# Kernel tuning notes

Hardware: AMD Instinct MI355X
Metric: run time of the kernel (lower is better)

Reference implementation:

```python
import jax, jax.numpy as jnp
import numpy as np

B, NINP, NCLS = 16384, 2048, 100


def setup_inputs() -> dict:
    key = jax.random.key(0)
    k1, k2, k3, k4, k5 = jax.random.split(key, 5)
    s = 1.0 / np.sqrt(NINP)
    return {
        "time_series": jax.random.normal(k1, (B, NINP), jnp.float32),
        "w_weight": jax.random.uniform(k2, (NINP, NINP), jnp.float32, -s, s),
        "w_bias": jax.random.uniform(k3, (NINP,), jnp.float32, -s, s),
        "fc_weight": jax.random.uniform(k4, (NCLS, NINP), jnp.float32, -s, s),
        "fc_bias": jax.random.uniform(k5, (NCLS,), jnp.float32, -s, s),
    }


def reference(time_series, w_weight, w_bias, fc_weight, fc_bias):
    # time_series: [B, N]
    n = time_series.shape[1]
    # gamma = cumsum(softmax(w(x), axis=1), axis=1): monotone warp in (0, 1]
    gamma = jnp.cumsum(jax.nn.softmax(time_series @ w_weight.T + w_bias, axis=1), axis=1)
    # Interp1d(linspace(0,1,N), x, gamma): per-row linear interpolation,
    # sampling each series at the warped time points gamma.
    xs = jnp.linspace(0.0, 1.0, n, dtype=time_series.dtype)  # shared knot grid
    warped = jax.vmap(lambda g, y: jnp.interp(g, xs, y))(gamma, time_series)  # [B, N]
    return warped @ fc_weight.T + fc_bias  # [B, nclasses]
```

## Files before the change

kernel.cpp:

```cpp
#include <hip/hip_runtime.h>
#include <hip/hip_bf16.h>

#define BROWS 16384
#define NDIM  2048
#define NCLS  100

typedef __attribute__((ext_vector_type(8))) __bf16 bf16x8;
typedef __attribute__((ext_vector_type(4))) float f32x4;
typedef __attribute__((ext_vector_type(16))) float f32x16;
typedef __attribute__((ext_vector_type(4))) unsigned short u16x4;
typedef __attribute__((ext_vector_type(8))) unsigned short u16x8;

__device__ __forceinline__ unsigned short f2bf(float f) {
    union { float f; unsigned int u; } v; v.f = f;
    unsigned int u = v.u;
    unsigned int r = (u + 0x7fffu + ((u >> 16) & 1u)) >> 16;
    return (unsigned short)r;
}
__device__ __forceinline__ float bf2f(unsigned short h) {
    union { unsigned int u; float f; } v; v.u = ((unsigned int)h) << 16;
    return v.f;
}

#define GLOAD_LDS(g, l) \
    __builtin_amdgcn_global_load_lds((const __attribute__((address_space(1))) void*)(g), \
                                     (__attribute__((address_space(3))) void*)(l), 16, 0, 0)

#define WAITCNT_VM(N) asm volatile("s_waitcnt vmcnt(" #N ")" ::: "memory")
#define WAITCNT_LGKM0() do { \
    asm volatile("s_waitcnt lgkmcnt(0)" ::: "memory"); \
    __builtin_amdgcn_sched_barrier(0); \
} while (0)
#define RAW_BARRIER() __builtin_amdgcn_s_barrier()

__global__ __launch_bounds__(256) void prep_kernel(const float4* __restrict__ x,
                                                   const float4* __restrict__ w,
                                                   u16x4* __restrict__ xhi, u16x4* __restrict__ xlo,
                                                   u16x4* __restrict__ whi, u16x4* __restrict__ wlo,
                                                   int n4x, int n4w)
{
    int i = blockIdx.x * 256 + threadIdx.x;
    const float4* src; u16x4 *hi, *lo; int idx;
    if (i < n4x) { src = x; hi = xhi; lo = xlo; idx = i; }
    else { idx = i - n4x; if (idx >= n4w) return; src = w; hi = whi; lo = wlo; }
    float4 v = src[idx];
    u16x4 h, l;
    h.x = f2bf(v.x); l.x = f2bf(v.x - bf2f(h.x));
    h.y = f2bf(v.y); l.y = f2bf(v.y - bf2f(h.y));
    h.z = f2bf(v.z); l.z = f2bf(v.z - bf2f(h.z));
    h.w = f2bf(v.w); l.w = f2bf(v.w - bf2f(h.w));
    hi[idx] = h; lo[idx] = l;
}

__global__ __launch_bounds__(256) void cvt_bf16_kernel(const float4* __restrict__ src,
                                                       u16x4* __restrict__ dst, int n4)
{
    int i = blockIdx.x * 256 + threadIdx.x;
    if (i >= n4) return;
    float4 v = src[i];
    u16x4 h;
    h.x = f2bf(v.x); h.y = f2bf(v.y); h.z = f2bf(v.z); h.w = f2bf(v.w);
    dst[i] = h;
}

__global__ __launch_bounds__(512) void gemm1_mfma_fused_kernel(
        const unsigned short* __restrict__ xhi,
        const unsigned short* __restrict__ xlo,
        const unsigned short* __restrict__ whi,
        const unsigned short* __restrict__ wlo,
        const float* __restrict__ bias,
        float* __restrict__ C)
{
    __shared__ unsigned short sAh[3 * 128 * 32];
    __shared__ unsigned short sAl[3 * 128 * 32];
    __shared__ unsigned short sBh[3 * 256 * 32];
    __shared__ unsigned short sBl[3 * 256 * 32];

    const int tid  = threadIdx.x;
    const int lane = tid & 63;
    const int w    = tid >> 6;
    const int wm   = w & 1;
    const int wn   = w >> 1;
    const int m0   = blockIdx.y * 128;
    const int n0   = blockIdx.x * 256;

    const int ra = tid >> 2;
    const int qa = (tid & 3) ^ ((ra >> 1) & 3);
    const size_t a_goff = (size_t)(m0 + ra) * NDIM + qa * 8;
    const int a_lb = (w * 64) * 8;

    size_t b_goff[2]; int b_lb[2];
#pragma unroll
    for (int t = 0; t < 2; t++) {
        const int c = t * 512 + tid;
        const int r = c >> 2;
        const int q = (c & 3) ^ ((r >> 1) & 3);
        b_goff[t] = (size_t)(n0 + r) * NDIM + q * 8;
        b_lb[t]   = (t * 512 + w * 64) * 8;
    }

    const int ln32 = lane & 31;
    const int lk2  = lane >> 5;
    int offA[2][2], offB[2][2];
#pragma unroll
    for (int i = 0; i < 2; i++)
#pragma unroll
        for (int ks = 0; ks < 2; ks++) {
            const int rfa = wm * 64 + i * 32 + ln32;
            offA[i][ks] = rfa * 32 + (((2 * ks + lk2) ^ ((rfa >> 1) & 3)) * 8);
            const int rfb = wn * 64 + i * 32 + ln32;
            offB[i][ks] = rfb * 32 + (((2 * ks + lk2) ^ ((rfb >> 1) & 3)) * 8);
        }

    f32x16 acc[2][2];
#pragma unroll
    for (int i = 0; i < 2; i++)
#pragma unroll
        for (int j = 0; j < 2; j++)
#pragma unroll
            for (int r = 0; r < 16; r++) acc[i][j][r] = 0.f;

#define G1_STAGE_ALL(AOFF, BOFF, KT) do { \
    GLOAD_LDS(xhi + a_goff + (KT), &sAh[(AOFF) + a_lb]); \
    GLOAD_LDS(xlo + a_goff + (KT), &sAl[(AOFF) + a_lb]); \
    GLOAD_LDS(whi + b_goff[0] + (KT), &sBh[(BOFF) + b_lb[0]]); \
    GLOAD_LDS(whi + b_goff[1] + (KT), &sBh[(BOFF) + b_lb[1]]); \
    GLOAD_LDS(wlo + b_goff[0] + (KT), &sBl[(BOFF) + b_lb[0]]); \
    GLOAD_LDS(wlo + b_goff[1] + (KT), &sBl[(BOFF) + b_lb[1]]); \
} while (0)

    G1_STAGE_ALL(0, 0, 0);
    G1_STAGE_ALL(4096, 8192, 32);
    WAITCNT_VM(6);
    RAW_BARRIER();

    int cA = 0, cB = 0;
    int sA = 2 * 4096, sB = 2 * 8192;

    for (int kt = 0; kt < NDIM; kt += 32) {
        const int skt = (kt + 64 < NDIM) ? kt + 64 : 0;

        {
            bf16x8 ah[2], al[2], bh[2], bl[2];
#pragma unroll
            for (int i = 0; i < 2; i++) {
                ah[i] = *(const bf16x8*)&sAh[cA + offA[i][0]];
                al[i] = *(const bf16x8*)&sAl[cA + offA[i][0]];
                bh[i] = *(const bf16x8*)&sBh[cB + offB[i][0]];
                bl[i] = *(const bf16x8*)&sBl[cB + offB[i][0]];
            }
            GLOAD_LDS(xhi + a_goff + skt, &sAh[sA + a_lb]);
            GLOAD_LDS(xlo + a_goff + skt, &sAl[sA + a_lb]);
            GLOAD_LDS(whi + b_goff[0] + skt, &sBh[sB + b_lb[0]]);
            RAW_BARRIER();
            WAITCNT_LGKM0();
            __builtin_amdgcn_s_setprio(1);
#pragma unroll
            for (int i = 0; i < 2; i++)
#pragma unroll
                for (int j = 0; j < 2; j++) {
                    acc[i][j] = __builtin_amdgcn_mfma_f32_32x32x16_bf16(ah[i], bh[j], acc[i][j], 0, 0, 0);
                    acc[i][j] = __builtin_amdgcn_mfma_f32_32x32x16_bf16(ah[i], bl[j], acc[i][j], 0, 0, 0);
                    acc[i][j] = __builtin_amdgcn_mfma_f32_32x32x16_bf16(al[i], bh[j], acc[i][j], 0, 0, 0);
                }
            __builtin_amdgcn_s_setprio(0);
            RAW_BARRIER();
        }

        {
            bf16x8 ah[2], al[2], bh[2], bl[2];
#pragma unroll
            for (int i = 0; i < 2; i++) {
                ah[i] = *(const bf16x8*)&sAh[cA + offA[i][1]];
                al[i] = *(const bf16x8*)&sAl[cA + offA[i][1]];
                bh[i] = *(const bf16x8*)&sBh[cB + offB[i][1]];
                bl[i] = *(const bf16x8*)&sBl[cB + offB[i][1]];
            }
            GLOAD_LDS(whi + b_goff[1] + skt, &sBh[sB + b_lb[1]]);
            GLOAD_LDS(wlo + b_goff[0] + skt, &sBl[sB + b_lb[0]]);
            GLOAD_LDS(wlo + b_goff[1] + skt, &sBl[sB + b_lb[1]]);
            WAITCNT_VM(6);
            RAW_BARRIER();
            WAITCNT_LGKM0();
            __builtin_amdgcn_s_setprio(1);
#pragma unroll
            for (int i = 0; i < 2; i++)
#pragma unroll
                for (int j = 0; j < 2; j++) {
                    acc[i][j] = __builtin_amdgcn_mfma_f32_32x32x16_bf16(ah[i], bh[j], acc[i][j], 0, 0, 0);
                    acc[i][j] = __builtin_amdgcn_mfma_f32_32x32x16_bf16(ah[i], bl[j], acc[i][j], 0, 0, 0);
                    acc[i][j] = __builtin_amdgcn_mfma_f32_32x32x16_bf16(al[i], bh[j], acc[i][j], 0, 0, 0);
                }
            __builtin_amdgcn_s_setprio(0);
            RAW_BARRIER();
        }

        cA += 4096; if (cA == 12288) cA = 0;
        cB += 8192; if (cB == 24576) cB = 0;
        sA += 4096; if (sA == 12288) sA = 0;
        sB += 8192; if (sB == 24576) sB = 0;
    }

#undef G1_STAGE_ALL

    float bb[2];
#pragma unroll
    for (int j = 0; j < 2; j++) bb[j] = bias[n0 + wn * 64 + j * 32 + ln32];
#pragma unroll
    for (int i = 0; i < 2; i++) {
#pragma unroll
        for (int j = 0; j < 2; j++) {
            const int n = n0 + wn * 64 + j * 32 + ln32;
#pragma unroll
            for (int reg = 0; reg < 16; reg++) {
                const int m = m0 + wm * 64 + i * 32 + (reg & 3) + 8 * (reg >> 2) + 4 * lk2;
                C[(size_t)m * NDIM + n] = acc[i][j][reg] + bb[j];
            }
        }
    }
}

#define SXI(i) ((i) + ((i) >> 5))

__global__ __launch_bounds__(256) void warp_bf16_kernel(const unsigned short* __restrict__ Xhi,
                                                        const unsigned short* __restrict__ Xlo,
                                                        const float* __restrict__ L,
                                                        unsigned short* __restrict__ Wout)
{
    const int N = NDIM;
    const int row = blockIdx.x;
    const int tid = threadIdx.x;
    const int lane = tid & 63;
    const int wave = tid >> 6;

    __shared__ float s_x[NDIM + NDIM / 32];
    __shared__ float s_red[4];
    __shared__ float s_wsum[4];

    const float* lrow = L + (size_t)row * N;

    float v[8];
    {
        float4 l0 = *(const float4*)(lrow + tid * 8);
        float4 l1 = *(const float4*)(lrow + tid * 8 + 4);
        v[0] = l0.x; v[1] = l0.y; v[2] = l0.z; v[3] = l0.w;
        v[4] = l1.x; v[5] = l1.y; v[6] = l1.z; v[7] = l1.w;
        u16x8 hx = *(const u16x8*)(Xhi + (size_t)row * N + tid * 8);
        u16x8 lx = *(const u16x8*)(Xlo + (size_t)row * N + tid * 8);
        float xv[8];
#pragma unroll
        for (int j = 0; j < 8; j++) xv[j] = bf2f(hx[j]) + bf2f(lx[j]);
        const int sb = SXI(tid * 8);
        *(float4*)&s_x[sb]     = make_float4(xv[0], xv[1], xv[2], xv[3]);
        *(float4*)&s_x[sb + 4] = make_float4(xv[4], xv[5], xv[6], xv[7]);
    }

    float mx = v[0];
#pragma unroll
    for (int j = 1; j < 8; j++) mx = fmaxf(mx, v[j]);
#pragma unroll
    for (int off = 32; off > 0; off >>= 1) mx = fmaxf(mx, __shfl_down(mx, off));
    if (lane == 0) s_red[wave] = mx;
    __syncthreads();
    mx = fmaxf(fmaxf(s_red[0], s_red[1]), fmaxf(s_red[2], s_red[3]));

    float c = 0.0f;
#pragma unroll
    for (int j = 0; j < 8; j++) {
        float e = __expf(v[j] - mx);
        c += e;
        v[j] = c;
    }

    float sc = c;
#pragma unroll
    for (int off = 1; off < 64; off <<= 1) {
        float t = __shfl_up(sc, off);
        if (lane >= off) sc += t;
    }
    if (lane == 63) s_wsum[wave] = sc;
    __syncthreads();
    float base = 0.0f, total = 0.0f;
#pragma unroll
    for (int w = 0; w < 4; w++) {
        float t = s_wsum[w];
        if (w < wave) base += t;
        total += t;
    }
    const float inv = 1.0f / total;
    const float prefix = base + (sc - c);

    u16x8 o;
#pragma unroll
    for (int j = 0; j < 8; j++) {
        float g = (prefix + v[j]) * inv;
        float pos = g * (float)(N - 1);
        pos = fminf(fmaxf(pos, 0.0f), (float)(N - 1));
        int i = (int)pos;
        if (i > N - 2) i = N - 2;
        float f = pos - (float)i;
        float x0 = s_x[SXI(i)];
        float x1 = s_x[SXI(i + 1)];
        o[j] = f2bf(fmaf(f, x1 - x0, x0));
    }
    *(u16x8*)(Wout + (size_t)row * N + tid * 8) = o;
}

__global__ __launch_bounds__(256) void gemm2_mfma_kernel(
        const unsigned short* __restrict__ Wp,
        const unsigned short* __restrict__ F,
        const float* __restrict__ fb,
        float* __restrict__ out)
{
    __shared__ unsigned short sA[2 * 32 * 64];
    __shared__ unsigned short sB[2 * 128 * 64];

    const int tid  = threadIdx.x;
    const int lane = tid & 63;
    const int w    = tid >> 6;
    const int m0   = blockIdx.x * 32;

    const int ar = tid >> 3, aq = tid & 7;
    const size_t a_goff = (size_t)(m0 + ar) * NDIM + ((aq ^ (ar & 7)) * 8);
    const int a_lb = (w * 64) * 8;

    size_t b_goff[4]; int b_lb[4];
#pragma unroll
    for (int t = 0; t < 4; t++) {
        const int c = t * 256 + tid;
        const int r = c >> 3, q = c & 7;
        b_goff[t] = (size_t)(r < NCLS ? r : NCLS - 1) * NDIM + ((q ^ (r & 7)) * 8);
        b_lb[t]   = (t * 256 + w * 64) * 8;
    }

    const int lm = lane & 15;
    const int lk = lane >> 4;
    int offA[2][2], offB[2][2];
#pragma unroll
    for (int i = 0; i < 2; i++)
#pragma unroll
        for (int ks = 0; ks < 2; ks++) {
            const int r = i * 16 + lm;
            offA[i][ks] = (r * 8 + ((ks * 4 + lk) ^ (r & 7))) * 8;
            const int rb = w * 32 + i * 16 + lm;
            offB[i][ks] = (rb * 8 + ((ks * 4 + lk) ^ (rb & 7))) * 8;
        }

    f32x4 acc[2][2];
#pragma unroll
    for (int i = 0; i < 2; i++)
#pragma unroll
        for (int j = 0; j < 2; j++) acc[i][j] = (f32x4){0.f, 0.f, 0.f, 0.f};

#define G2_STAGE(B, KT) do { \
    GLOAD_LDS(Wp + a_goff + (KT), &sA[(B) * 2048 + a_lb]); \
    _Pragma("unroll") \
    for (int t = 0; t < 4; t++) GLOAD_LDS(F + b_goff[t] + (KT), &sB[(B) * 8192 + b_lb[t]]); \
} while (0)

#define G2_COMPUTE(B) do { \
    _Pragma("unroll") \
    for (int ks = 0; ks < 2; ks++) { \
        bf16x8 af[2], bfr[2]; \
        _Pragma("unroll") \
        for (int i = 0; i < 2; i++) { \
            af[i]  = *(const bf16x8*)&sA[(B) * 2048 + offA[i][ks]]; \
            bfr[i] = *(const bf16x8*)&sB[(B) * 8192 + offB[i][ks]]; \
        } \
        _Pragma("unroll") \
        for (int i = 0; i < 2; i++) \
            _Pragma("unroll") \
            for (int j = 0; j < 2; j++) \
                acc[i][j] = __builtin_amdgcn_mfma_f32_16x16x32_bf16(af[i], bfr[j], acc[i][j], 0, 0, 0); \
    } \
} while (0)

    G2_STAGE(0, 0);

    for (int kt = 0; kt < NDIM; kt += 128) {
        G2_STAGE(1, kt + 64);
        WAITCNT_VM(5);
        RAW_BARRIER();
        G2_COMPUTE(0);
        RAW_BARRIER();
        G2_STAGE(0, (kt + 128 < NDIM) ? kt + 128 : 0);
        WAITCNT_VM(5);
        RAW_BARRIER();
        G2_COMPUTE(1);
        RAW_BARRIER();
    }

#undef G2_STAGE
#undef G2_COMPUTE

    const int cn = lane & 15;
    const int rg = lane >> 4;
#pragma unroll
    for (int i = 0; i < 2; i++) {
#pragma unroll
        for (int j = 0; j < 2; j++) {
            const int n = w * 32 + j * 16 + cn;
            if (n < NCLS) {
                const float bbn = fb[n];
#pragma unroll
                for (int reg = 0; reg < 4; reg++) {
                    const int m = m0 + i * 16 + rg * 4 + reg;
                    out[(size_t)m * NCLS + n] = acc[i][j][reg] + bbn;
                }
            }
        }
    }
}

__global__ __launch_bounds__(256) void gemm1_kernel(const float* __restrict__ X,
                                                    const float* __restrict__ W,
                                                    const float* __restrict__ bias,
                                                    float* __restrict__ C)
{
    const int K = NDIM;
    __shared__ float sA[16][128];
    __shared__ float sB[16][128];
    const int tid = threadIdx.x;
    const int tx = tid & 15;
    const int ty = tid >> 4;
    const int m0 = blockIdx.y * 128;
    const int n0 = blockIdx.x * 128;
    float acc[8][8];
#pragma unroll
    for (int i = 0; i < 8; i++)
#pragma unroll
        for (int j = 0; j < 8; j++) acc[i][j] = 0.0f;
    const int s_m = tid >> 1;
    const int s_c = (tid & 1) * 8;
    const float* Ag = X + (size_t)(m0 + s_m) * K + s_c;
    const float* Bg = W + (size_t)(n0 + s_m) * K + s_c;
    for (int kt = 0; kt < K; kt += 16) {
        float4 av0 = *(const float4*)(Ag + kt);
        float4 av1 = *(const float4*)(Ag + kt + 4);
        float4 bv0 = *(const float4*)(Bg + kt);
        float4 bv1 = *(const float4*)(Bg + kt + 4);
        __syncthreads();
        sA[s_c + 0][s_m] = av0.x; sA[s_c + 1][s_m] = av0.y;
        sA[s_c + 2][s_m] = av0.z; sA[s_c + 3][s_m] = av0.w;
        sA[s_c + 4][s_m] = av1.x; sA[s_c + 5][s_m] = av1.y;
        sA[s_c + 6][s_m] = av1.z; sA[s_c + 7][s_m] = av1.w;
        sB[s_c + 0][s_m] = bv0.x; sB[s_c + 1][s_m] = bv0.y;
        sB[s_c + 2][s_m] = bv0.z; sB[s_c + 3][s_m] = bv0.w;
        sB[s_c + 4][s_m] = bv1.x; sB[s_c + 5][s_m] = bv1.y;
        sB[s_c + 6][s_m] = bv1.z; sB[s_c + 7][s_m] = bv1.w;
        __syncthreads();
#pragma unroll
        for (int k = 0; k < 16; k++) {
            float4 a0 = *(const float4*)&sA[k][ty * 8];
            float4 a1 = *(const float4*)&sA[k][ty * 8 + 4];
            float4 b0 = *(const float4*)&sB[k][tx * 8];
            float4 b1 = *(const float4*)&sB[k][tx * 8 + 4];
            float a[8] = {a0.x, a0.y, a0.z, a0.w, a1.x, a1.y, a1.z, a1.w};
            float b[8] = {b0.x, b0.y, b0.z, b0.w, b1.x, b1.y, b1.z, b1.w};
#pragma unroll
            for (int i = 0; i < 8; i++)
#pragma unroll
                for (int j = 0; j < 8; j++)
                    acc[i][j] = fmaf(a[i], b[j], acc[i][j]);
        }
    }
    float bb[8];
#pragma unroll
    for (int j = 0; j < 8; j++) bb[j] = bias[n0 + tx * 8 + j];
#pragma unroll
    for (int i = 0; i < 8; i++) {
        const int m = m0 + ty * 8 + i;
        float* crow = C + (size_t)m * NDIM + n0 + tx * 8;
        *(float4*)(crow)     = make_float4(acc[i][0] + bb[0], acc[i][1] + bb[1],
                                           acc[i][2] + bb[2], acc[i][3] + bb[3]);
        *(float4*)(crow + 4) = make_float4(acc[i][4] + bb[4], acc[i][5] + bb[5],
                                           acc[i][6] + bb[6], acc[i][7] + bb[7]);
    }
}

__global__ __launch_bounds__(256) void warp_kernel_f32(const float* __restrict__ X,
                                                       float* __restrict__ L)
{
    const int N = NDIM;
    const int row = blockIdx.x;
    const int tid = threadIdx.x;
    const int lane = tid & 63;
    const int wave = tid >> 6;
    __shared__ float s_x[NDIM];
    __shared__ float s_red[4];
    __shared__ float s_wsum[4];
    float* lrow = L + (size_t)row * N;
    const float* xrow = X + (size_t)row * N;
    float v[8];
    {
        float4 l0 = *(const float4*)(lrow + tid * 8);
        float4 l1 = *(const float4*)(lrow + tid * 8 + 4);
        v[0] = l0.x; v[1] = l0.y; v[2] = l0.z; v[3] = l0.w;
        v[4] = l1.x; v[5] = l1.y; v[6] = l1.z; v[7] = l1.w;
        float4 x0 = *(const float4*)(xrow + tid * 8);
        float4 x1 = *(const float4*)(xrow + tid * 8 + 4);
        *(float4*)&s_x[tid * 8]     = x0;
        *(float4*)&s_x[tid * 8 + 4] = x1;
    }
    float mx = v[0];
#pragma unroll
    for (int j = 1; j < 8; j++) mx = fmaxf(mx, v[j]);
#pragma unroll
    for (int off = 32; off > 0; off >>= 1) mx = fmaxf(mx, __shfl_down(mx, off));
    if (lane == 0) s_red[wave] = mx;
    __syncthreads();
    mx = fmaxf(fmaxf(s_red[0], s_red[1]), fmaxf(s_red[2], s_red[3]));
    float c = 0.0f;
#pragma unroll
    for (int j = 0; j < 8; j++) {
        float e = __expf(v[j] - mx);
        c += e;
        v[j] = c;
    }
    float sc = c;
#pragma unroll
    for (int off = 1; off < 64; off <<= 1) {
        float t = __shfl_up(sc, off);
        if (lane >= off) sc += t;
    }
    if (lane == 63) s_wsum[wave] = sc;
    __syncthreads();
    float base = 0.0f, total = 0.0f;
#pragma unroll
    for (int w = 0; w < 4; w++) {
        float t = s_wsum[w];
        if (w < wave) base += t;
        total += t;
    }
    const float inv = 1.0f / total;
    const float prefix = base + (sc - c);
    float w8[8];
#pragma unroll
    for (int j = 0; j < 8; j++) {
        float g = (prefix + v[j]) * inv;
        float pos = g * (float)(N - 1);
        pos = fminf(fmaxf(pos, 0.0f), (float)(N - 1));
        int i = (int)pos;
        if (i > N - 2) i = N - 2;
        float f = pos - (float)i;
        w8[j] = fmaf(f, s_x[i + 1] - s_x[i], s_x[i]);
    }
    *(float4*)(lrow + tid * 8)     = make_float4(w8[0], w8[1], w8[2], w8[3]);
    *(float4*)(lrow + tid * 8 + 4) = make_float4(w8[4], w8[5], w8[6], w8[7]);
}

__global__ __launch_bounds__(256) void gemm2_kernel(const float* __restrict__ Wp,
                                                    const float* __restrict__ F,
                                                    const float* __restrict__ fb,
                                                    float* __restrict__ out)
{
    const int K = NDIM;
    __shared__ float sA[16][64];
    __shared__ float sB[16][128];
    const int tid = threadIdx.x;
    const int tx = tid & 15;
    const int ty = tid >> 4;
    const int m0 = blockIdx.x * 64;
    float acc[4][8];
#pragma unroll
    for (int i = 0; i < 4; i++)
#pragma unroll
        for (int j = 0; j < 8; j++) acc[i][j] = 0.0f;
    const int a_m = tid >> 2;
    const int a_c = (tid & 3) * 4;
    const int b_n = tid >> 1;
    const int b_c = (tid & 1) * 8;
    const bool bvalid = (b_n < NCLS);
    const float* Ag = Wp + (size_t)(m0 + a_m) * K + a_c;
    const float* Bg = F + (size_t)b_n * K + b_c;
    for (int kt = 0; kt < K; kt += 16) {
        float4 av = *(const float4*)(Ag + kt);
        float4 bv0 = make_float4(0.f, 0.f, 0.f, 0.f);
        float4 bv1 = make_float4(0.f, 0.f, 0.f, 0.f);
        if (bvalid) {
            bv0 = *(const float4*)(Bg + kt);
            bv1 = *(const float4*)(Bg + kt + 4);
        }
        __syncthreads();
        sA[a_c + 0][a_m] = av.x; sA[a_c + 1][a_m] = av.y;
        sA[a_c + 2][a_m] = av.z; sA[a_c + 3][a_m] = av.w;
        sB[b_c + 0][b_n] = bv0.x; sB[b_c + 1][b_n] = bv0.y;
        sB[b_c + 2][b_n] = bv0.z; sB[b_c + 3][b_n] = bv0.w;
        sB[b_c + 4][b_n] = bv1.x; sB[b_c + 5][b_n] = bv1.y;
        sB[b_c + 6][b_n] = bv1.z; sB[b_c + 7][b_n] = bv1.w;
        __syncthreads();
#pragma unroll
        for (int k = 0; k < 16; k++) {
            float4 a4 = *(const float4*)&sA[k][ty * 4];
            float4 b0 = *(const float4*)&sB[k][tx * 8];
            float4 b1 = *(const float4*)&sB[k][tx * 8 + 4];
            float a[4] = {a4.x, a4.y, a4.z, a4.w};
            float b[8] = {b0.x, b0.y, b0.z, b0.w, b1.x, b1.y, b1.z, b1.w};
#pragma unroll
            for (int i = 0; i < 4; i++)
#pragma unroll
                for (int j = 0; j < 8; j++)
                    acc[i][j] = fmaf(a[i], b[j], acc[i][j]);
        }
    }
#pragma unroll
    for (int i = 0; i < 4; i++) {
        const int m = m0 + ty * 4 + i;
#pragma unroll
        for (int j = 0; j < 8; j++) {
            const int n = tx * 8 + j;
            if (n < NCLS) out[(size_t)m * NCLS + n] = acc[i][j] + fb[n];
        }
    }
}

extern "C" void kernel_launch(void* const* d_in, const int* in_sizes, int n_in,
                              void* d_out, int out_size, void* d_ws, size_t ws_size,
                              hipStream_t stream) {
    const float* x  = (const float*)d_in[0];
    const float* ww = (const float*)d_in[1];
    const float* wb = (const float*)d_in[2];
    const float* fw = (const float*)d_in[3];
    const float* fb = (const float*)d_in[4];
    float* out = (float*)d_out;

    char* ws = (char*)d_ws;
    float* logits = (float*)ws;
    const size_t LOGITS_B = (size_t)BROWS * NDIM * 4;
    const size_t XBF_B    = (size_t)BROWS * NDIM * 2;
    const size_t WBF_B    = (size_t)NDIM * NDIM * 2;
    unsigned short* xhi = (unsigned short*)(ws + LOGITS_B);
    unsigned short* xlo = (unsigned short*)(ws + LOGITS_B + XBF_B);
    unsigned short* whi = (unsigned short*)(ws + LOGITS_B + 2 * XBF_B);
    unsigned short* wlo = (unsigned short*)(ws + LOGITS_B + 2 * XBF_B + WBF_B);
    unsigned short* wbf = xlo;
    unsigned short* fwb = wlo;
    const size_t WS_NEED = LOGITS_B + 2 * XBF_B + 2 * WBF_B;

    if (ws_size >= WS_NEED) {
        const int n4x = BROWS * NDIM / 4;
        const int n4w = NDIM * NDIM / 4;
        prep_kernel<<<(n4x + n4w + 255) / 256, 256, 0, stream>>>(
            (const float4*)x, (const float4*)ww,
            (u16x4*)xhi, (u16x4*)xlo, (u16x4*)whi, (u16x4*)wlo, n4x, n4w);
        gemm1_mfma_fused_kernel<<<dim3(NDIM / 256, BROWS / 128), 512, 0, stream>>>(
            xhi, xlo, whi, wlo, wb, logits);
        warp_bf16_kernel<<<BROWS, 256, 0, stream>>>(xhi, xlo, logits, wbf);
        cvt_bf16_kernel<<<(NCLS * NDIM / 4 + 255) / 256, 256, 0, stream>>>(
            (const float4*)fw, (u16x4*)fwb, NCLS * NDIM / 4);
        gemm2_mfma_kernel<<<BROWS / 32, 256, 0, stream>>>(wbf, fwb, fb, out);
    } else {
        gemm1_kernel<<<dim3(NDIM / 128, BROWS / 128), 256, 0, stream>>>(x, ww, wb, logits);
        warp_kernel_f32<<<BROWS, 256, 0, stream>>>(x, logits);
        gemm2_kernel<<<BROWS / 64, 256, 0, stream>>>(logits, fw, fb, out);
    }
}
```

Baseline: 664.9 us.

## Fuse softmax-cumsum warp interpolation into the second GEMM kernel

Merges the per-row softmax/cumsum/interpolation kernel into the classifier GEMM. Each block warps 16 rows, one wave per row at a time, and writes the bf16 results straight into a padded LDS A-tile. The MFMA loop then streams only the fc weights. This removes the global write and re-read of the warped bf16 matrix and one kernel launch. In exchange it uses large LDS (about 100KB per block), lowering occupancy. The warp phase is serialized per wave, and fc weights are reloaded by twice as many blocks.

```diff
diff --git a/kernel.cpp b/kernel.cpp
--- a/kernel.cpp
+++ b/kernel.cpp
@@ -220,109 +220,98 @@
     }
 }
 
-#define SXI(i) ((i) + ((i) >> 5))
-
-__global__ __launch_bounds__(256) void warp_bf16_kernel(const unsigned short* __restrict__ Xhi,
-                                                        const unsigned short* __restrict__ Xlo,
-                                                        const float* __restrict__ L,
-                                                        unsigned short* __restrict__ Wout)
-{
-    const int N = NDIM;
-    const int row = blockIdx.x;
-    const int tid = threadIdx.x;
-    const int lane = tid & 63;
-    const int wave = tid >> 6;
-
-    __shared__ float s_x[NDIM + NDIM / 32];
-    __shared__ float s_red[4];
-    __shared__ float s_wsum[4];
-
-    const float* lrow = L + (size_t)row * N;
-
-    float v[8];
-    {
-        float4 l0 = *(const float4*)(lrow + tid * 8);
-        float4 l1 = *(const float4*)(lrow + tid * 8 + 4);
-        v[0] = l0.x; v[1] = l0.y; v[2] = l0.z; v[3] = l0.w;
-        v[4] = l1.x; v[5] = l1.y; v[6] = l1.z; v[7] = l1.w;
-        u16x8 hx = *(const u16x8*)(Xhi + (size_t)row * N + tid * 8);
-        u16x8 lx = *(const u16x8*)(Xlo + (size_t)row * N + tid * 8);
-        float xv[8];
-#pragma unroll
-        for (int j = 0; j < 8; j++) xv[j] = bf2f(hx[j]) + bf2f(lx[j]);
-        const int sb = SXI(tid * 8);
-        *(float4*)&s_x[sb]     = make_float4(xv[0], xv[1], xv[2], xv[3]);
-        *(float4*)&s_x[sb + 4] = make_float4(xv[4], xv[5], xv[6], xv[7]);
-    }
-
-    float mx = v[0];
-#pragma unroll
-    for (int j = 1; j < 8; j++) mx = fmaxf(mx, v[j]);
-#pragma unroll
-    for (int off = 32; off > 0; off >>= 1) mx = fmaxf(mx, __shfl_down(mx, off));
-    if (lane == 0) s_red[wave] = mx;
-    __syncthreads();
-    mx = fmaxf(fmaxf(s_red[0], s_red[1]), fmaxf(s_red[2], s_red[3]));
-
-    float c = 0.0f;
-#pragma unroll
-    for (int j = 0; j < 8; j++) {
-        float e = __expf(v[j] - mx);
-        c += e;
-        v[j] = c;
-    }
-
-    float sc = c;
-#pragma unroll
-    for (int off = 1; off < 64; off <<= 1) {
-        float t = __shfl_up(sc, off);
-        if (lane >= off) sc += t;
-    }
-    if (lane == 63) s_wsum[wave] = sc;
-    __syncthreads();
-    float base = 0.0f, total = 0.0f;
-#pragma unroll
-    for (int w = 0; w < 4; w++) {
-        float t = s_wsum[w];
-        if (w < wave) base += t;
-        total += t;
-    }
-    const float inv = 1.0f / total;
-    const float prefix = base + (sc - c);
-
-    u16x8 o;
-#pragma unroll
-    for (int j = 0; j < 8; j++) {
-        float g = (prefix + v[j]) * inv;
-        float pos = g * (float)(N - 1);
-        pos = fminf(fmaxf(pos, 0.0f), (float)(N - 1));
-        int i = (int)pos;
-        if (i > N - 2) i = N - 2;
-        float f = pos - (float)i;
-        float x0 = s_x[SXI(i)];
-        float x1 = s_x[SXI(i + 1)];
-        o[j] = f2bf(fmaf(f, x1 - x0, x0));
-    }
-    *(u16x8*)(Wout + (size_t)row * N + tid * 8) = o;
-}
-
-__global__ __launch_bounds__(256) void gemm2_mfma_kernel(
-        const unsigned short* __restrict__ Wp,
+#define APAD 2056
+
+__global__ __launch_bounds__(256) void fused_warp_gemm2_kernel(
+        const unsigned short* __restrict__ Xhi,
+        const unsigned short* __restrict__ Xlo,
+        const float* __restrict__ L,
         const unsigned short* __restrict__ F,
         const float* __restrict__ fb,
         float* __restrict__ out)
 {
-    __shared__ unsigned short sA[2 * 32 * 64];
+    __shared__ unsigned short sA[16 * APAD];
+    __shared__ float s_x[4 * 2112];
     __shared__ unsigned short sB[2 * 128 * 64];
 
     const int tid  = threadIdx.x;
     const int lane = tid & 63;
     const int w    = tid >> 6;
-    const int m0   = blockIdx.x * 32;
-
-    const int ar = tid >> 3, aq = tid & 7;
-    const size_t a_goff = (size_t)(m0 + ar) * NDIM + ((aq ^ (ar & 7)) * 8);
-    const int a_lb = (w * 64) * 8;
+    const int m0   = blockIdx.x * 16;
+
+    {
+        float* sx = &s_x[w * 2112];
+        for (int rr = 0; rr < 4; rr++) {
+            const int arow = w * 4 + rr;
+            const size_t grow = (size_t)(m0 + arow) * NDIM;
+            const float* lrow = L + grow;
+            const unsigned short* hrow = Xhi + grow;
+            const unsigned short* orow = Xlo + grow;
+            const int e0 = lane * 32;
+
+            float v[32];
+#pragma unroll
+            for (int q = 0; q < 8; q++) {
+                float4 t = *(const float4*)(lrow + e0 + q * 4);
+                v[q * 4 + 0] = t.x; v[q * 4 + 1] = t.y;
+                v[q * 4 + 2] = t.z; v[q * 4 + 3] = t.w;
+            }
+            {
+                const int sb = e0 + lane;
+#pragma unroll
+                for (int q = 0; q < 4; q++) {
+                    u16x8 hx = *(const u16x8*)(hrow + e0 + q * 8);
+                    u16x8 lx = *(const u16x8*)(orow + e0 + q * 8);
+#pragma unroll
+                    for (int j = 0; j < 8; j++)
+                        sx[sb + q * 8 + j] = bf2f(hx[j]) + bf2f(lx[j]);
+                }
+            }
+
+            float mx = v[0];
+#pragma unroll
+            for (int j = 1; j < 32; j++) mx = fmaxf(mx, v[j]);
+#pragma unroll
+            for (int off = 32; off > 0; off >>= 1)
+                mx = fmaxf(mx, __shfl_xor(mx, off));
+
+            float c = 0.0f;
+#pragma unroll
+            for (int j = 0; j < 32; j++) {
+                float e = __expf(v[j] - mx);
+                c += e;
+                v[j] = c;
+            }
+            float sc = c;
+#pragma unroll
+            for (int off = 1; off < 64; off <<= 1) {
+                float t = __shfl_up(sc, off);
+                if (lane >= off) sc += t;
+            }
+            const float total = __shfl(sc, 63);
+            const float inv = 1.0f / total;
+            const float prefix = sc - c;
+
+            unsigned short* arowp = &sA[arow * APAD + e0];
+#pragma unroll
+            for (int q = 0; q < 4; q++) {
+                u16x8 o;
+#pragma unroll
+                for (int j = 0; j < 8; j++) {
+                    float g = (prefix + v[q * 8 + j]) * inv;
+                    float pos = fminf(fmaxf(g * (float)(NDIM - 1), 0.0f), (float)(NDIM - 1));
+                    int i = (int)pos;
+                    if (i > NDIM - 2) i = NDIM - 2;
+                    float f = pos - (float)i;
+                    float x0 = sx[i + (i >> 5)];
+                    float x1 = sx[(i + 1) + ((i + 1) >> 5)];
+                    o[j] = f2bf(fmaf(f, x1 - x0, x0));
+                }
+                *(u16x8*)(arowp + q * 8) = o;
+            }
+        }
+    }
+    __syncthreads();
 
     size_t b_goff[4]; int b_lb[4];
 #pragma unroll
@@ -335,78 +324,66 @@
 
     const int lm = lane & 15;
     const int lk = lane >> 4;
-    int offA[2][2], offB[2][2];
-#pragma unroll
-    for (int i = 0; i < 2; i++)
+    int offB[2][2];
+#pragma unroll
+    for (int j = 0; j < 2; j++)
 #pragma unroll
         for (int ks = 0; ks < 2; ks++) {
-            const int r = i * 16 + lm;
-            offA[i][ks] = (r * 8 + ((ks * 4 + lk) ^ (r & 7))) * 8;
-            const int rb = w * 32 + i * 16 + lm;
-            offB[i][ks] = (rb * 8 + ((ks * 4 + lk) ^ (rb & 7))) * 8;
-        }
-
-    f32x4 acc[2][2];
-#pragma unroll
-    for (int i = 0; i < 2; i++)
-#pragma unroll
-        for (int j = 0; j < 2; j++) acc[i][j] = (f32x4){0.f, 0.f, 0.f, 0.f};
-
-#define G2_STAGE(B, KT) do { \
-    GLOAD_LDS(Wp + a_goff + (KT), &sA[(B) * 2048 + a_lb]); \
+            const int r = w * 32 + j * 16 + lm;
+            offB[j][ks] = (r * 8 + ((ks * 4 + lk) ^ (r & 7))) * 8;
+        }
+    const int aoff = lm * APAD + lk * 8;
+
+    f32x4 acc[2];
+    acc[0] = (f32x4){0.f, 0.f, 0.f, 0.f};
+    acc[1] = (f32x4){0.f, 0.f, 0.f, 0.f};
+
+#define FG_STAGE(B, KT) do { \
     _Pragma("unroll") \
     for (int t = 0; t < 4; t++) GLOAD_LDS(F + b_goff[t] + (KT), &sB[(B) * 8192 + b_lb[t]]); \
 } while (0)
 
-#define G2_COMPUTE(B) do { \
+#define FG_COMPUTE(B, KTA) do { \
     _Pragma("unroll") \
     for (int ks = 0; ks < 2; ks++) { \
-        bf16x8 af[2], bfr[2]; \
+        bf16x8 af = *(const bf16x8*)&sA[aoff + (KTA) + ks * 32]; \
         _Pragma("unroll") \
-        for (int i = 0; i < 2; i++) { \
-            af[i]  = *(const bf16x8*)&sA[(B) * 2048 + offA[i][ks]]; \
-            bfr[i] = *(const bf16x8*)&sB[(B) * 8192 + offB[i][ks]]; \
+        for (int j = 0; j < 2; j++) { \
+            bf16x8 bfr = *(const bf16x8*)&sB[(B) * 8192 + offB[j][ks]]; \
+            acc[j] = __builtin_amdgcn_mfma_f32_16x16x32_bf16(af, bfr, acc[j], 0, 0, 0); \
         } \
-        _Pragma("unroll") \
-        for (int i = 0; i < 2; i++) \
-            _Pragma("unroll") \
-            for (int j = 0; j < 2; j++) \
-                acc[i][j] = __builtin_amdgcn_mfma_f32_16x16x32_bf16(af[i], bfr[j], acc[i][j], 0, 0, 0); \
     } \
 } while (0)
 
-    G2_STAGE(0, 0);
+    FG_STAGE(0, 0);
 
     for (int kt = 0; kt < NDIM; kt += 128) {
-        G2_STAGE(1, kt + 64);
-        WAITCNT_VM(5);
+        FG_STAGE(1, kt + 64);
+        WAITCNT_VM(4);
         RAW_BARRIER();
-        G2_COMPUTE(0);
+        FG_COMPUTE(0, kt);
         RAW_BARRIER();
-        G2_STAGE(0, (kt + 128 < NDIM) ? kt + 128 : 0);
-        WAITCNT_VM(5);
+        FG_STAGE(0, (kt + 128 < NDIM) ? kt + 128 : 0);
+        WAITCNT_VM(4);
         RAW_BARRIER();
-        G2_COMPUTE(1);
+        FG_COMPUTE(1, kt + 64);
         RAW_BARRIER();
     }
 
-#undef G2_STAGE
-#undef G2_COMPUTE
+#undef FG_STAGE
+#undef FG_COMPUTE
 
     const int cn = lane & 15;
     const int rg = lane >> 4;
 #pragma unroll
-    for (int i = 0; i < 2; i++) {
-#pragma unroll
-        for (int j = 0; j < 2; j++) {
-            const int n = w * 32 + j * 16 + cn;
-            if (n < NCLS) {
-                const float bbn = fb[n];
-#pragma unroll
-                for (int reg = 0; reg < 4; reg++) {
-                    const int m = m0 + i * 16 + rg * 4 + reg;
-                    out[(size_t)m * NCLS + n] = acc[i][j][reg] + bbn;
-                }
+    for (int j = 0; j < 2; j++) {
+        const int n = w * 32 + j * 16 + cn;
+        if (n < NCLS) {
+            const float bbn = fb[n];
+#pragma unroll
+            for (int reg = 0; reg < 4; reg++) {
+                const int m = m0 + rg * 4 + reg;
+                out[(size_t)m * NCLS + n] = acc[j][reg] + bbn;
             }
         }
     }
@@ -633,7 +610,6 @@
     unsigned short* xlo = (unsigned short*)(ws + LOGITS_B + XBF_B);
     unsigned short* whi = (unsigned short*)(ws + LOGITS_B + 2 * XBF_B);
     unsigned short* wlo = (unsigned short*)(ws + LOGITS_B + 2 * XBF_B + WBF_B);
-    unsigned short* wbf = xlo;
     unsigned short* fwb = wlo;
     const size_t WS_NEED = LOGITS_B + 2 * XBF_B + 2 * WBF_B;
 
@@ -645,10 +621,10 @@
             (u16x4*)xhi, (u16x4*)xlo, (u16x4*)whi, (u16x4*)wlo, n4x, n4w);
         gemm1_mfma_fused_kernel<<<dim3(NDIM / 256, BROWS / 128), 512, 0, stream>>>(
             xhi, xlo, whi, wlo, wb, logits);
-        warp_bf16_kernel<<<BROWS, 256, 0, stream>>>(xhi, xlo, logits, wbf);
         cvt_bf16_kernel<<<(NCLS * NDIM / 4 + 255) / 256, 256, 0, stream>>>(
             (const float4*)fw, (u16x4*)fwb, NCLS * NDIM / 4);
-        gemm2_mfma_kernel<<<BROWS / 32, 256, 0, stream>>>(wbf, fwb, fb, out);
+        fused_warp_gemm2_kernel<<<BROWS / 16, 256, 0, stream>>>(
+            xhi, xlo, logits, fwb, fb, out);
     } else {
         gemm1_kernel<<<dim3(NDIM / 128, BROWS / 128), 256, 0, stream>>>(x, ww, wb, logits);
         warp_kernel_f32<<<BROWS, 256, 0, stream>>>(x, logits);
```

New measurement: 706.7 us. +6.3%, slower.

## Shrink gemm2 row tile to 16 and load A fragments directly from global

Applied to the files above, without the earlier changes.

The second GEMM (warped activations times fc weight) now uses 16-row tiles instead of 32, doubling the grid to 1024 blocks, and reads A fragments straight from global memory into registers instead of staging them through LDS. This removes the A LDS buffer and its async copies, and raises block count for better CU occupancy on this small-N GEMM. In exchange the fc-weight tile in LDS is reloaded by twice as many blocks, and each wave's A loads are uncoalesced 16-byte reads.

```diff
diff --git a/kernel.cpp b/kernel.cpp
--- a/kernel.cpp
+++ b/kernel.cpp
@@ -312,17 +312,12 @@
         const float* __restrict__ fb,
         float* __restrict__ out)
 {
-    __shared__ unsigned short sA[2 * 32 * 64];
     __shared__ unsigned short sB[2 * 128 * 64];
 
     const int tid  = threadIdx.x;
     const int lane = tid & 63;
     const int w    = tid >> 6;
-    const int m0   = blockIdx.x * 32;
-
-    const int ar = tid >> 3, aq = tid & 7;
-    const size_t a_goff = (size_t)(m0 + ar) * NDIM + ((aq ^ (ar & 7)) * 8);
-    const int a_lb = (w * 64) * 8;
+    const int m0   = blockIdx.x * 16;
 
     size_t b_goff[4]; int b_lb[4];
 #pragma unroll
@@ -335,78 +330,63 @@
 
     const int lm = lane & 15;
     const int lk = lane >> 4;
-    int offA[2][2], offB[2][2];
-#pragma unroll
-    for (int i = 0; i < 2; i++)
+    int offB[2][2];
+#pragma unroll
+    for (int j = 0; j < 2; j++)
 #pragma unroll
         for (int ks = 0; ks < 2; ks++) {
-            const int r = i * 16 + lm;
-            offA[i][ks] = (r * 8 + ((ks * 4 + lk) ^ (r & 7))) * 8;
-            const int rb = w * 32 + i * 16 + lm;
-            offB[i][ks] = (rb * 8 + ((ks * 4 + lk) ^ (rb & 7))) * 8;
-        }
-
-    f32x4 acc[2][2];
-#pragma unroll
-    for (int i = 0; i < 2; i++)
-#pragma unroll
-        for (int j = 0; j < 2; j++) acc[i][j] = (f32x4){0.f, 0.f, 0.f, 0.f};
+            const int r = w * 32 + j * 16 + lm;
+            offB[j][ks] = (r * 8 + ((ks * 4 + lk) ^ (r & 7))) * 8;
+        }
+    const unsigned short* aptr = Wp + (size_t)(m0 + lm) * NDIM + lk * 8;
+
+    f32x4 acc[2];
+    acc[0] = (f32x4){0.f, 0.f, 0.f, 0.f};
+    acc[1] = (f32x4){0.f, 0.f, 0.f, 0.f};
 
 #define G2_STAGE(B, KT) do { \
-    GLOAD_LDS(Wp + a_goff + (KT), &sA[(B) * 2048 + a_lb]); \
     _Pragma("unroll") \
     for (int t = 0; t < 4; t++) GLOAD_LDS(F + b_goff[t] + (KT), &sB[(B) * 8192 + b_lb[t]]); \
 } while (0)
 
-#define G2_COMPUTE(B) do { \
+#define G2_ITER(CURB, NXTB, KT) do { \
+    bf16x8 a0 = *(const bf16x8*)(aptr + (KT));               \
+    bf16x8 a1 = *(const bf16x8*)(aptr + (KT) + 32);          \
+    const int nkt = ((KT) + 64 < NDIM) ? (KT) + 64 : 0;      \
+    G2_STAGE(NXTB, nkt); \
+    WAITCNT_VM(4);           \
+    RAW_BARRIER(); \
     _Pragma("unroll") \
-    for (int ks = 0; ks < 2; ks++) { \
-        bf16x8 af[2], bfr[2]; \
-        _Pragma("unroll") \
-        for (int i = 0; i < 2; i++) { \
-            af[i]  = *(const bf16x8*)&sA[(B) * 2048 + offA[i][ks]]; \
-            bfr[i] = *(const bf16x8*)&sB[(B) * 8192 + offB[i][ks]]; \
-        } \
-        _Pragma("unroll") \
-        for (int i = 0; i < 2; i++) \
-            _Pragma("unroll") \
-            for (int j = 0; j < 2; j++) \
-                acc[i][j] = __builtin_amdgcn_mfma_f32_16x16x32_bf16(af[i], bfr[j], acc[i][j], 0, 0, 0); \
+    for (int j = 0; j < 2; j++) { \
+        bf16x8 b0 = *(const bf16x8*)&sB[(CURB) * 8192 + offB[j][0]]; \
+        acc[j] = __builtin_amdgcn_mfma_f32_16x16x32_bf16(a0, b0, acc[j], 0, 0, 0); \
+        bf16x8 b1 = *(const bf16x8*)&sB[(CURB) * 8192 + offB[j][1]]; \
+        acc[j] = __builtin_amdgcn_mfma_f32_16x16x32_bf16(a1, b1, acc[j], 0, 0, 0); \
     } \
+    RAW_BARRIER(); \
 } while (0)
 
     G2_STAGE(0, 0);
 
     for (int kt = 0; kt < NDIM; kt += 128) {
-        G2_STAGE(1, kt + 64);
-        WAITCNT_VM(5);
-        RAW_BARRIER();
-        G2_COMPUTE(0);
-        RAW_BARRIER();
-        G2_STAGE(0, (kt + 128 < NDIM) ? kt + 128 : 0);
-        WAITCNT_VM(5);
-        RAW_BARRIER();
-        G2_COMPUTE(1);
-        RAW_BARRIER();
+        G2_ITER(0, 1, kt);
+        G2_ITER(1, 0, kt + 64);
     }
 
 #undef G2_STAGE
-#undef G2_COMPUTE
+#undef G2_ITER
 
     const int cn = lane & 15;
     const int rg = lane >> 4;
 #pragma unroll
-    for (int i = 0; i < 2; i++) {
-#pragma unroll
-        for (int j = 0; j < 2; j++) {
-            const int n = w * 32 + j * 16 + cn;
-            if (n < NCLS) {
-                const float bbn = fb[n];
-#pragma unroll
-                for (int reg = 0; reg < 4; reg++) {
-                    const int m = m0 + i * 16 + rg * 4 + reg;
-                    out[(size_t)m * NCLS + n] = acc[i][j][reg] + bbn;
-                }
+    for (int j = 0; j < 2; j++) {
+        const int n = w * 32 + j * 16 + cn;
+        if (n < NCLS) {
+            const float bbn = fb[n];
+#pragma unroll
+            for (int reg = 0; reg < 4; reg++) {
+                const int m = m0 + rg * 4 + reg;
+                out[(size_t)m * NCLS + n] = acc[j][reg] + bbn;
             }
         }
     }
@@ -648,7 +628,7 @@
         warp_bf16_kernel<<<BROWS, 256, 0, stream>>>(xhi, xlo, logits, wbf);
         cvt_bf16_kernel<<<(NCLS * NDIM / 4 + 255) / 256, 256, 0, stream>>>(
             (const float4*)fw, (u16x4*)fwb, NCLS * NDIM / 4);
-        gemm2_mfma_kernel<<<BROWS / 32, 256, 0, stream>>>(wbf, fwb, fb, out);
+        gemm2_mfma_kernel<<<BROWS / 16, 256, 0, stream>>>(wbf, fwb, fb, out);
     } else {
         gemm1_kernel<<<dim3(NDIM / 128, BROWS / 128), 256, 0, stream>>>(x, ww, wb, logits);
         warp_kernel_f32<<<BROWS, 256, 0, stream>>>(x, logits);
```

After: 701.9 us. +5.6%, slower.
